# Optimization experiments

Measured on AMD Instinct MI355X. Metric: run time of the kernel, lower is better.

## Reference

```python
import jax, jax.numpy as jnp
import numpy as np

N = 50000      # nodes
E = 800000     # edges (before self-loops)
IN = 128       # in_channels
HID = 32       # hidden_channels
H = 4          # num_heads
OUT = 2        # out_channels
NEG_SLOPE = 0.2


def setup_inputs() -> dict:
    key = jax.random.key(0)
    ks = jax.random.split(key, 16)
    s = 0.1
    x = jax.random.normal(ks[0], (N, IN), jnp.float32)
    edge_index = jax.random.randint(ks[1], (2, E), 0, N, dtype=jnp.int32)
    W1 = jax.random.normal(ks[2], (IN, H * HID), jnp.float32) * s
    att_src1 = jax.random.normal(ks[3], (H, HID), jnp.float32) * s
    att_dst1 = jax.random.normal(ks[4], (H, HID), jnp.float32) * s
    b1 = jnp.zeros((H * HID,), jnp.float32)
    W2 = jax.random.normal(ks[5], (H * HID, H * HID), jnp.float32) * s
    att_src2 = jax.random.normal(ks[6], (H, HID), jnp.float32) * s
    att_dst2 = jax.random.normal(ks[7], (H, HID), jnp.float32) * s
    b2 = jnp.zeros((H * HID,), jnp.float32)
    W3 = jax.random.normal(ks[8], (H * HID, OUT), jnp.float32) * s
    att_src3 = jax.random.normal(ks[9], (1, OUT), jnp.float32) * s
    att_dst3 = jax.random.normal(ks[10], (1, OUT), jnp.float32) * s
    b3 = jnp.zeros((OUT,), jnp.float32)
    return {"x": x, "edge_index": edge_index,
            "W1": W1, "att_src1": att_src1, "att_dst1": att_dst1, "b1": b1,
            "W2": W2, "att_src2": att_src2, "att_dst2": att_dst2, "b2": b2,
            "W3": W3, "att_src3": att_src3, "att_dst3": att_dst3, "b3": b3}


def gat_layer(x, src, dst, W, a_src, a_dst, b, heads, ch, concat):
    """PyG GATConv (eval mode): per-edge LeakyReLU attention, edge-softmax over
    incoming edges of each destination node, weighted scatter-add aggregation."""
    n = x.shape[0]
    h = (x @ W).reshape(n, heads, ch)                      # [N,H,C]
    alpha_s = jnp.sum(h * a_src, axis=-1)                  # [N,H]
    alpha_d = jnp.sum(h * a_dst, axis=-1)                  # [N,H]
    alpha = jax.nn.leaky_relu(alpha_s[src] + alpha_d[dst], NEG_SLOPE)  # [E',H]
    amax = jax.ops.segment_max(alpha, dst, num_segments=n)             # [N,H]
    e = jnp.exp(alpha - amax[dst])
    denom = jax.ops.segment_sum(e, dst, num_segments=n)
    w = e / denom[dst]                                     # softmax weights [E',H]
    out = jax.ops.segment_sum(h[src] * w[:, :, None], dst, num_segments=n)  # [N,H,C]
    out = out.reshape(n, heads * ch) if concat else out.mean(axis=1)
    return out + b


def reference(x, edge_index, W1, att_src1, att_dst1, b1,
              W2, att_src2, att_dst2, b2, W3, att_src3, att_dst3, b3):
    # PyG GATConv adds self-loops by default
    loop = jnp.arange(N, dtype=edge_index.dtype)
    src = jnp.concatenate([edge_index[0], loop])
    dst = jnp.concatenate([edge_index[1], loop])
    h = jax.nn.elu(gat_layer(x, src, dst, W1, att_src1, att_dst1, b1, H, HID, True))
    h = jax.nn.elu(gat_layer(h, src, dst, W2, att_src2, att_dst2, b2, H, HID, True))
    h = gat_layer(h, src, dst, W3, att_src3, att_dst3, b3, 1, OUT, False)
    return jax.nn.log_softmax(h, axis=1)
```

## Files before the change

### kernel.cpp

```cpp
#include <hip/hip_runtime.h>
#include <hip/hip_fp16.h>

#define NN 50000
#define EE 800000
#define ET 850000
#define NEG 0.2f
#define SCAN_B 1024
#define NBLK ((NN + SCAN_B - 1) / SCAN_B)

__device__ __forceinline__ float leaky(float x) { return fmaxf(x, NEG * x); }
__device__ __forceinline__ float elu_f(float x) { return x > 0.f ? x : expm1f(x); }

struct alignas(8) half4 { __half2 a, b; };

typedef _Float16 half8_t __attribute__((ext_vector_type(8)));
typedef float float4_t __attribute__((ext_vector_type(4)));

__global__ void hist_k(const int* __restrict__ ei, int* __restrict__ counts,
                       int* __restrict__ rank) {
    int i = blockIdx.x * blockDim.x + threadIdx.x;
    if (i >= ET) return;
    int dst = (i < EE) ? __builtin_nontemporal_load(ei + EE + i) : (i - EE);
    int r = atomicAdd(&counts[dst], 1);
    __builtin_nontemporal_store(r, rank + i);
}

__global__ void scan1_k(const int* __restrict__ counts, int* __restrict__ rp,
                        int* __restrict__ bsums) {
    __shared__ int lsum[256];
    int base = blockIdx.x * SCAN_B;
    int v[4];
    int tsum = 0;
#pragma unroll
    for (int j = 0; j < 4; ++j) {
        int i = base + threadIdx.x * 4 + j;
        v[j] = (i < NN) ? counts[i] : 0;
        tsum += v[j];
    }
    lsum[threadIdx.x] = tsum;
    __syncthreads();
    for (int off = 1; off < 256; off <<= 1) {
        int t = (threadIdx.x >= off) ? lsum[threadIdx.x - off] : 0;
        __syncthreads();
        lsum[threadIdx.x] += t;
        __syncthreads();
    }
    int excl = lsum[threadIdx.x] - tsum;
#pragma unroll
    for (int j = 0; j < 4; ++j) {
        int i = base + threadIdx.x * 4 + j;
        if (i < NN) rp[i] = excl;
        excl += v[j];
    }
    if (threadIdx.x == 255) bsums[blockIdx.x] = lsum[255];
}

__global__ void scan2_k(int* __restrict__ bsums, int* __restrict__ rp) {
    int lane = threadIdx.x;
    int v = (lane < NBLK) ? bsums[lane] : 0;
    int orig = v;
    for (int off = 1; off < 64; off <<= 1) {
        int t = __shfl_up(v, off, 64);
        if (lane >= off) v += t;
    }
    if (lane < NBLK) bsums[lane] = v - orig;
    if (lane == 63) rp[NN] = v;
}

__global__ void scan3_k(int* __restrict__ rp, const int* __restrict__ bsums) {
    int add = bsums[blockIdx.x];
    int base = blockIdx.x * SCAN_B + threadIdx.x * 4;
#pragma unroll
    for (int j = 0; j < 4; ++j) {
        int i = base + j;
        if (i < NN) rp[i] += add;
    }
}

__global__ void scatter_k(const int* __restrict__ ei, const int* __restrict__ rp,
                          const int* __restrict__ rank, int* __restrict__ csr) {
    int i = blockIdx.x * blockDim.x + threadIdx.x;
    if (i >= ET) return;
    int src, dst;
    if (i < EE) {
        src = __builtin_nontemporal_load(ei + i);
        dst = __builtin_nontemporal_load(ei + EE + i);
    } else {
        src = dst = i - EE;
    }
    int r = __builtin_nontemporal_load(rank + i);
    csr[rp[dst] + r] = src;
}

__global__ void wt_k(const float* __restrict__ W1, const float* __restrict__ W2,
                     __half* __restrict__ Wt1, __half* __restrict__ Wt2) {
    int i = blockIdx.x * 256 + threadIdx.x;
    const float* W = (i < 16384) ? W1 : W2;
    __half* Wt = (i < 16384) ? Wt1 : Wt2;
    int j = i & 16383;
    int k = j >> 7, n = j & 127;
    Wt[n * 128 + k] = __float2half(W[j]);
}

__global__ __launch_bounds__(256)
void gemm_mfma_k(const float* __restrict__ Xf, const __half* __restrict__ Xh,
                 const __half* __restrict__ Wt, __half* __restrict__ Yh, int nrows,
                 const float* __restrict__ att_s, const float* __restrict__ att_d,
                 float* __restrict__ asb, float* __restrict__ adb) {
    __shared__ __align__(16) __half cst[4][16 * 128];
    int lane = threadIdx.x & 63;
    int wid  = threadIdx.x >> 6;
    int n = lane & 15, quad = lane >> 4;
    int row0 = (blockIdx.x * 4 + wid) * 16;

    float atts_r[8], attd_r[8];
#pragma unroll
    for (int t = 0; t < 8; ++t) {
        atts_r[t] = att_s[t * 16 + n];
        attd_r[t] = att_d[t * 16 + n];
    }

    float4_t acc[8];
#pragma unroll
    for (int t = 0; t < 8; ++t) acc[t] = (float4_t){0.f, 0.f, 0.f, 0.f};
    int rA = row0 + n; if (rA >= nrows) rA = nrows - 1;
#pragma unroll
    for (int ch = 0; ch < 4; ++ch) {
        half8_t a;
        if (Xh) {
            a = __builtin_nontemporal_load(
                    (const half8_t*)(Xh + (size_t)rA * 128 + ch * 32 + quad * 8));
        } else {
            const float4_t* xp = (const float4_t*)(Xf + (size_t)rA * 128 + ch * 32 + quad * 8);
            float4_t f0 = __builtin_nontemporal_load(xp);
            float4_t f1 = __builtin_nontemporal_load(xp + 1);
            a = (half8_t){(_Float16)f0.x, (_Float16)f0.y, (_Float16)f0.z, (_Float16)f0.w,
                          (_Float16)f1.x, (_Float16)f1.y, (_Float16)f1.z, (_Float16)f1.w};
        }
#pragma unroll
        for (int t = 0; t < 8; ++t) {
            half8_t b = *(const half8_t*)(Wt + (t * 16 + n) * 128 + ch * 32 + quad * 8);
            acc[t] = __builtin_amdgcn_mfma_f32_16x16x32_f16(a, b, acc[t], 0, 0, 0);
        }
    }

#pragma unroll
    for (int rg = 0; rg < 4; ++rg) {
        float ps[4], pd[4];
#pragma unroll
        for (int h = 0; h < 4; ++h) {
            ps[h] = acc[2*h][rg] * atts_r[2*h] + acc[2*h+1][rg] * atts_r[2*h+1];
            pd[h] = acc[2*h][rg] * attd_r[2*h] + acc[2*h+1][rg] * attd_r[2*h+1];
#pragma unroll
            for (int mask = 1; mask < 16; mask <<= 1) {
                ps[h] += __shfl_xor(ps[h], mask, 64);
                pd[h] += __shfl_xor(pd[h], mask, 64);
            }
        }
        int row = row0 + quad * 4 + rg;
        if (n == 0 && row < nrows) {
#pragma unroll
            for (int h = 0; h < 4; ++h) {
                asb[row * 4 + h] = ps[h];
                adb[row * 4 + h] = pd[h];
            }
        }
    }

#pragma unroll
    for (int rg = 0; rg < 4; ++rg)
#pragma unroll
        for (int t = 0; t < 8; ++t)
            cst[wid][(quad * 4 + rg) * 128 + t * 16 + n] = __float2half(acc[t][rg]);
    __syncthreads();
    {
        int chunk = lane & 15;
        int rsub  = lane >> 4;
#pragma unroll
        for (int it = 0; it < 4; ++it) {
            int row = it * 4 + rsub;
            int grow = row0 + row;
            if (grow < nrows) {
                half8_t v = *(const half8_t*)(&cst[wid][row * 128 + chunk * 8]);
                *(half8_t*)(Yh + (size_t)grow * 128 + chunk * 8) = v;
            }
        }
    }
}

__global__ __launch_bounds__(256)
void agg_k(const __half* __restrict__ Hh, const float* __restrict__ asb,
           const float* __restrict__ adb, const int* __restrict__ rp,
           const int* __restrict__ csr, const float* __restrict__ bias,
           __half* __restrict__ Y,
           const float* __restrict__ W3, const float* __restrict__ s3w,
           const float* __restrict__ d3w, float* __restrict__ h3,
           float* __restrict__ as3, float* __restrict__ ad3) {
    int lane = threadIdx.x & 63;
    int hw = lane >> 5;
    int l  = lane & 31;
    int n = blockIdx.x * 8 + (threadIdx.x >> 6) * 2 + hw;
    if (n >= NN) return;
    int hd = l >> 3;
    float ad = adb[n * 4 + hd];
    float acc0 = 0.f, acc1 = 0.f, acc2 = 0.f, acc3 = 0.f, den = 0.f;
    int e = rp[n], end = rp[n + 1], last = end - 1;
    for (int base = e; base < end; base += 16) {
        int s[16]; float a[16]; float2 hraw[16];
#pragma unroll
        for (int j = 0; j < 16; ++j) {
            int i = base + j;
            s[j] = csr[i <= last ? i : last];
        }
#pragma unroll
        for (int j = 0; j < 16; ++j) a[j] = asb[s[j] * 4 + hd] + ad;
#pragma unroll
        for (int j = 0; j < 16; ++j)
            hraw[j] = ((const float2*)(Hh + (size_t)s[j] * 128))[l];
#pragma unroll
        for (int j = 0; j < 16; ++j) {
            float w = __expf(leaky(a[j]));
            w = (base + j <= last) ? w : 0.f;
            den += w;
            const __half2* hp = (const __half2*)&hraw[j];
            float2 f01 = __half22float2(hp[0]);
            float2 f23 = __half22float2(hp[1]);
            acc0 += w * f01.x; acc1 += w * f01.y;
            acc2 += w * f23.x; acc3 += w * f23.y;
        }
    }
    float4 bv = ((const float4*)bias)[l];
    float inv = 1.f / den;
    float o0 = elu_f(acc0 * inv + bv.x);
    float o1 = elu_f(acc1 * inv + bv.y);
    float o2 = elu_f(acc2 * inv + bv.z);
    float o3 = elu_f(acc3 * inv + bv.w);
    if (!W3) {
        half4 hv;
        hv.a = __floats2half2_rn(o0, o1);
        hv.b = __floats2half2_rn(o2, o3);
        ((half4*)(Y + (size_t)n * 128))[l] = hv;
    } else {
        float4 wa = ((const float4*)W3)[l * 2];
        float4 wb = ((const float4*)W3)[l * 2 + 1];
        float p0 = o0 * wa.x + o1 * wa.z + o2 * wb.x + o3 * wb.z;
        float p1 = o0 * wa.y + o1 * wa.w + o2 * wb.y + o3 * wb.w;
        for (int off = 16; off > 0; off >>= 1) {
            p0 += __shfl_down(p0, off, 32);
            p1 += __shfl_down(p1, off, 32);
        }
        if (l == 0) {
            h3[n * 2 + 0] = p0;
            h3[n * 2 + 1] = p1;
            as3[n] = p0 * s3w[0] + p1 * s3w[1];
            ad3[n] = p0 * d3w[0] + p1 * d3w[1];
        }
    }
}

__global__ void l3agg_k(const float* __restrict__ h3, const float* __restrict__ as3,
                        const float* __restrict__ ad3, const int* __restrict__ rp,
                        const int* __restrict__ csr, const float* __restrict__ b3,
                        float* __restrict__ out) {
    int n = blockIdx.x * blockDim.x + threadIdx.x;
    if (n >= NN) return;
    const float2* h2 = (const float2*)h3;
    float adn = ad3[n];
    float den = 0.f, a0 = 0.f, a1 = 0.f;
    int e = rp[n], end = rp[n + 1], last = end - 1;
    for (int base = e; base < end; base += 4) {
        int s[4]; float al[4]; float2 g[4];
#pragma unroll
        for (int j = 0; j < 4; ++j) {
            int i = base + j;
            s[j] = csr[i <= last ? i : last];
        }
#pragma unroll
        for (int j = 0; j < 4; ++j) al[j] = as3[s[j]] + adn;
#pragma unroll
        for (int j = 0; j < 4; ++j) g[j] = h2[s[j]];
#pragma unroll
        for (int j = 0; j < 4; ++j) {
            float w = __expf(leaky(al[j]));
            w = (base + j <= last) ? w : 0.f;
            den += w;
            a0 += w * g[j].x;
            a1 += w * g[j].y;
        }
    }
    float o0 = a0 / den + b3[0];
    float o1 = a1 / den + b3[1];
    float m = fmaxf(o0, o1);
    float lse = m + logf(__expf(o0 - m) + __expf(o1 - m));
    out[n * 2 + 0] = o0 - lse;
    out[n * 2 + 1] = o1 - lse;
}

extern "C" void kernel_launch(void* const* d_in, const int* in_sizes, int n_in,
                              void* d_out, int out_size, void* d_ws, size_t ws_size,
                              hipStream_t stream) {
    const float* x   = (const float*)d_in[0];
    const int*   ei  = (const int*)d_in[1];
    const float* W1  = (const float*)d_in[2];
    const float* as1 = (const float*)d_in[3];
    const float* ad1 = (const float*)d_in[4];
    const float* b1  = (const float*)d_in[5];
    const float* W2  = (const float*)d_in[6];
    const float* as2 = (const float*)d_in[7];
    const float* ad2 = (const float*)d_in[8];
    const float* b2  = (const float*)d_in[9];
    const float* W3  = (const float*)d_in[10];
    const float* s3w = (const float*)d_in[11];
    const float* d3w = (const float*)d_in[12];
    const float* b3  = (const float*)d_in[13];
    float* out = (float*)d_out;

    char* ws = (char*)d_ws;
    size_t off = 0;
    auto alloc = [&](size_t bytes) -> char* {
        char* p = ws + off;
        off = (off + bytes + 255) & ~(size_t)255;
        return p;
    };
    __half* hA    = (__half*)alloc((size_t)NN * 128 * 2);
    __half* hBh   = (__half*)alloc((size_t)NN * 128 * 2);
    float* asb    = (float*)alloc((size_t)NN * 4 * 4);
    float* adb    = (float*)alloc((size_t)NN * 4 * 4);
    int*   rp     = (int*)alloc((size_t)(NN + 1) * 4);
    int*   counts = (int*)alloc((size_t)NN * 4);
    int*   csr    = (int*)alloc((size_t)ET * 4);
    int*   rank   = (int*)alloc((size_t)ET * 4);
    int*   bsums  = (int*)alloc((size_t)NBLK * 4);
    __half* Wt1   = (__half*)alloc(128 * 128 * 2);
    __half* Wt2   = (__half*)alloc(128 * 128 * 2);
    float* h3     = (float*)alloc((size_t)NN * 2 * 4);
    float* s3     = (float*)alloc((size_t)NN * 4);
    float* d3     = (float*)alloc((size_t)NN * 4);

    wt_k<<<128, 256, 0, stream>>>(W1, W2, Wt1, Wt2);

    hipMemsetAsync(counts, 0, (size_t)NN * 4, stream);
    hist_k<<<(ET + 255) / 256, 256, 0, stream>>>(ei, counts, rank);
    scan1_k<<<NBLK, 256, 0, stream>>>(counts, rp, bsums);
    scan2_k<<<1, 64, 0, stream>>>(bsums, rp);
    scan3_k<<<NBLK, 256, 0, stream>>>(rp, bsums);
    scatter_k<<<(ET + 255) / 256, 256, 0, stream>>>(ei, rp, rank, csr);

    gemm_mfma_k<<<(NN + 63) / 64, 256, 0, stream>>>(x, nullptr, Wt1, hA, NN,
                                                    as1, ad1, asb, adb);
    agg_k<<<(NN + 7) / 8, 256, 0, stream>>>(hA, asb, adb, rp, csr, b1, hBh,
                                            nullptr, nullptr, nullptr,
                                            nullptr, nullptr, nullptr);

    gemm_mfma_k<<<(NN + 63) / 64, 256, 0, stream>>>(nullptr, hBh, Wt2, hA, NN,
                                                    as2, ad2, asb, adb);
    agg_k<<<(NN + 7) / 8, 256, 0, stream>>>(hA, asb, adb, rp, csr, b2, nullptr,
                                            W3, s3w, d3w, h3, s3, d3);

    l3agg_k<<<(NN + 255) / 256, 256, 0, stream>>>(h3, s3, d3, rp, csr, b3, out);
}
```

Measured before the change: 306.0 us.

## Precompute per-edge attention weights in separate kernel before aggregation

Splits edge weight computation (leaky-relu + exp of src/dst attention logits) into a new ew_k kernel that writes per-edge float4 weights. The aggregation kernel then reads these precomputed weights instead of gathering asb and computing exp per lane, and its unroll depth drops from 16 to 8. The aim is to stop 32 lanes redundantly computing the same exp and to shorten the dependent gather chain, at the cost of an extra kernel launch and a 13.6 MB write plus read of the edge-weight buffer.

```diff
diff --git a/kernel.cpp b/kernel.cpp
--- a/kernel.cpp
+++ b/kernel.cpp
@@ -189,10 +189,30 @@
 }
 
 __global__ __launch_bounds__(256)
-void agg_k(const __half* __restrict__ Hh, const float* __restrict__ asb,
-           const float* __restrict__ adb, const int* __restrict__ rp,
-           const int* __restrict__ csr, const float* __restrict__ bias,
-           __half* __restrict__ Y,
+void ew_k(const int* __restrict__ rp, const int* __restrict__ csr,
+          const float* __restrict__ asb, const float* __restrict__ adb,
+          float* __restrict__ we) {
+    int n = blockIdx.x * 4 + (threadIdx.x >> 6);
+    if (n >= NN) return;
+    int lane = threadIdx.x & 63;
+    float4 ad = ((const float4*)adb)[n];
+    int e1 = rp[n + 1];
+    for (int e = rp[n] + lane; e < e1; e += 64) {
+        int s = csr[e];
+        float4 as = ((const float4*)asb)[s];
+        float4 w;
+        w.x = __expf(leaky(as.x + ad.x));
+        w.y = __expf(leaky(as.y + ad.y));
+        w.z = __expf(leaky(as.z + ad.z));
+        w.w = __expf(leaky(as.w + ad.w));
+        ((float4*)we)[e] = w;
+    }
+}
+
+__global__ __launch_bounds__(256)
+void agg_k(const __half* __restrict__ Hh, const float* __restrict__ we,
+           const int* __restrict__ rp, const int* __restrict__ csr,
+           const float* __restrict__ bias, __half* __restrict__ Y,
            const float* __restrict__ W3, const float* __restrict__ s3w,
            const float* __restrict__ d3w, float* __restrict__ h3,
            float* __restrict__ as3, float* __restrict__ ad3) {
@@ -202,25 +222,23 @@
     int n = blockIdx.x * 8 + (threadIdx.x >> 6) * 2 + hw;
     if (n >= NN) return;
     int hd = l >> 3;
-    float ad = adb[n * 4 + hd];
     float acc0 = 0.f, acc1 = 0.f, acc2 = 0.f, acc3 = 0.f, den = 0.f;
     int e = rp[n], end = rp[n + 1], last = end - 1;
-    for (int base = e; base < end; base += 16) {
-        int s[16]; float a[16]; float2 hraw[16];
-#pragma unroll
-        for (int j = 0; j < 16; ++j) {
+    for (int base = e; base < end; base += 8) {
+        int s[8]; float wv[8]; float2 hraw[8];
+#pragma unroll
+        for (int j = 0; j < 8; ++j) {
             int i = base + j;
-            s[j] = csr[i <= last ? i : last];
-        }
-#pragma unroll
-        for (int j = 0; j < 16; ++j) a[j] = asb[s[j] * 4 + hd] + ad;
-#pragma unroll
-        for (int j = 0; j < 16; ++j)
+            int ic = i <= last ? i : last;
+            s[j] = csr[ic];
+            wv[j] = we[ic * 4 + hd];
+        }
+#pragma unroll
+        for (int j = 0; j < 8; ++j)
             hraw[j] = ((const float2*)(Hh + (size_t)s[j] * 128))[l];
 #pragma unroll
-        for (int j = 0; j < 16; ++j) {
-            float w = __expf(leaky(a[j]));
-            w = (base + j <= last) ? w : 0.f;
+        for (int j = 0; j < 8; ++j) {
+            float w = (base + j <= last) ? wv[j] : 0.f;
             den += w;
             const __half2* hp = (const __half2*)&hraw[j];
             float2 f01 = __half22float2(hp[0]);
@@ -326,6 +344,7 @@
     __half* hBh   = (__half*)alloc((size_t)NN * 128 * 2);
     float* asb    = (float*)alloc((size_t)NN * 4 * 4);
     float* adb    = (float*)alloc((size_t)NN * 4 * 4);
+    float* we     = (float*)alloc((size_t)ET * 4 * 4);
     int*   rp     = (int*)alloc((size_t)(NN + 1) * 4);
     int*   counts = (int*)alloc((size_t)NN * 4);
     int*   csr    = (int*)alloc((size_t)ET * 4);
@@ -339,7 +358,7 @@
 
     wt_k<<<128, 256, 0, stream>>>(W1, W2, Wt1, Wt2);
 
-    hipMemsetAsync(counts, 0, (size_t)NN * 4, stream);
+    (void)hipMemsetAsync(counts, 0, (size_t)NN * 4, stream);
     hist_k<<<(ET + 255) / 256, 256, 0, stream>>>(ei, counts, rank);
     scan1_k<<<NBLK, 256, 0, stream>>>(counts, rp, bsums);
     scan2_k<<<1, 64, 0, stream>>>(bsums, rp);
@@ -348,13 +367,15 @@
 
     gemm_mfma_k<<<(NN + 63) / 64, 256, 0, stream>>>(x, nullptr, Wt1, hA, NN,
                                                     as1, ad1, asb, adb);
-    agg_k<<<(NN + 7) / 8, 256, 0, stream>>>(hA, asb, adb, rp, csr, b1, hBh,
+    ew_k<<<(NN + 3) / 4, 256, 0, stream>>>(rp, csr, asb, adb, we);
+    agg_k<<<(NN + 7) / 8, 256, 0, stream>>>(hA, we, rp, csr, b1, hBh,
                                             nullptr, nullptr, nullptr,
                                             nullptr, nullptr, nullptr);
 
     gemm_mfma_k<<<(NN + 63) / 64, 256, 0, stream>>>(nullptr, hBh, Wt2, hA, NN,
                                                     as2, ad2, asb, adb);
-    agg_k<<<(NN + 7) / 8, 256, 0, stream>>>(hA, asb, adb, rp, csr, b2, nullptr,
+    ew_k<<<(NN + 3) / 4, 256, 0, stream>>>(rp, csr, asb, adb, we);
+    agg_k<<<(NN + 7) / 8, 256, 0, stream>>>(hA, we, rp, csr, b2, nullptr,
                                             W3, s3w, d3w, h3, s3, d3);
 
     l3agg_k<<<(NN + 255) / 256, 256, 0, stream>>>(h3, s3, d3, rp, csr, b3, out);
```

Result: no change. 311.6 us (+1.8%).
